# Kernel optimization log

Hardware: AMD Instinct MI355X
Metric: run time of the kernel (lower is better)

Reference implementation:

```python
import jax, jax.numpy as jnp
import numpy as np

T, B, I, H = 512, 64, 256, 512

def setup_inputs() -> dict:
    key = jax.random.key(0)
    ks = jax.random.split(key, 5)
    s = 0.1  # matches uniform(-0.1, 0.1) init scale
    return {
        "x": jax.random.normal(ks[0], (T, B, I), dtype=jnp.float32),
        "weight_ih": jax.random.uniform(ks[1], (H, I), dtype=jnp.float32, minval=-s, maxval=s),
        "weight_hh": jax.random.uniform(ks[2], (H, H), dtype=jnp.float32, minval=-s, maxval=s),
        "bias_ih": jax.random.uniform(ks[3], (H,), dtype=jnp.float32, minval=-s, maxval=s),
        "bias_hh": jax.random.uniform(ks[4], (H,), dtype=jnp.float32, minval=-s, maxval=s),
    }

def reference(x, weight_ih, weight_hh, bias_ih, bias_hh):
    # Precompute input contribution for all timesteps in one big GEMM: [T,B,H]
    xw = jnp.einsum('tbi,hi->tbh', x, weight_ih) + bias_ih + bias_hh
    h0 = jnp.zeros((x.shape[1], weight_hh.shape[0]), dtype=x.dtype)

    def step(h, xw_t):
        h = jax.nn.relu(xw_t + h @ weight_hh.T)
        return h, h

    h_final, output = jax.lax.scan(step, h0, xw)
    return output, h_final
```

## Files before the change

### kernel.cpp

```cpp
#include <hip/hip_runtime.h>

#define T_DIM 512
#define B_DIM 64
#define I_DIM 256
#define H_DIM 512
#define BH_DIM (B_DIM * H_DIM)

__global__ __launch_bounds__(256) void xw_gemm(
    const float* __restrict__ x, const float* __restrict__ wih,
    const float* __restrict__ bih, const float* __restrict__ bhh,
    float* __restrict__ out) {
  __shared__ float xs[32][68];
  __shared__ float ws[32][68];

  const int m_base = blockIdx.y * 64;
  const int n_base = blockIdx.x * 64;
  const int tid = threadIdx.x;
  const int tn = tid & 15;
  const int tm = tid >> 4;
  const int lr = tid >> 3;
  const int lk = (tid & 7) << 2;

  float acc[4][4];
#pragma unroll
  for (int i = 0; i < 4; i++)
#pragma unroll
    for (int j = 0; j < 4; j++) acc[i][j] = 0.f;

  for (int kc = 0; kc < I_DIM; kc += 32) {
    __syncthreads();
    const float4 xv0 = *(const float4*)&x[(size_t)(m_base + lr) * I_DIM + kc + lk];
    const float4 xv1 = *(const float4*)&x[(size_t)(m_base + lr + 32) * I_DIM + kc + lk];
    const float4 wv0 = *(const float4*)&wih[(size_t)(n_base + lr) * I_DIM + kc + lk];
    const float4 wv1 = *(const float4*)&wih[(size_t)(n_base + lr + 32) * I_DIM + kc + lk];
    xs[lk + 0][lr] = xv0.x; xs[lk + 1][lr] = xv0.y;
    xs[lk + 2][lr] = xv0.z; xs[lk + 3][lr] = xv0.w;
    xs[lk + 0][lr + 32] = xv1.x; xs[lk + 1][lr + 32] = xv1.y;
    xs[lk + 2][lr + 32] = xv1.z; xs[lk + 3][lr + 32] = xv1.w;
    ws[lk + 0][lr] = wv0.x; ws[lk + 1][lr] = wv0.y;
    ws[lk + 2][lr] = wv0.z; ws[lk + 3][lr] = wv0.w;
    ws[lk + 0][lr + 32] = wv1.x; ws[lk + 1][lr + 32] = wv1.y;
    ws[lk + 2][lr + 32] = wv1.z; ws[lk + 3][lr + 32] = wv1.w;
    __syncthreads();

#pragma unroll
    for (int k = 0; k < 32; k++) {
      const float4 a = *(const float4*)&xs[k][tm * 4];
      const float4 b = *(const float4*)&ws[k][tn * 4];
      acc[0][0] = fmaf(a.x, b.x, acc[0][0]); acc[0][1] = fmaf(a.x, b.y, acc[0][1]);
      acc[0][2] = fmaf(a.x, b.z, acc[0][2]); acc[0][3] = fmaf(a.x, b.w, acc[0][3]);
      acc[1][0] = fmaf(a.y, b.x, acc[1][0]); acc[1][1] = fmaf(a.y, b.y, acc[1][1]);
      acc[1][2] = fmaf(a.y, b.z, acc[1][2]); acc[1][3] = fmaf(a.y, b.w, acc[1][3]);
      acc[2][0] = fmaf(a.z, b.x, acc[2][0]); acc[2][1] = fmaf(a.z, b.y, acc[2][1]);
      acc[2][2] = fmaf(a.z, b.z, acc[2][2]); acc[2][3] = fmaf(a.z, b.w, acc[2][3]);
      acc[3][0] = fmaf(a.w, b.x, acc[3][0]); acc[3][1] = fmaf(a.w, b.y, acc[3][1]);
      acc[3][2] = fmaf(a.w, b.z, acc[3][2]); acc[3][3] = fmaf(a.w, b.w, acc[3][3]);
    }
  }

  const int n0 = n_base + tn * 4;
  float4 bias;
  bias.x = bih[n0 + 0] + bhh[n0 + 0];
  bias.y = bih[n0 + 1] + bhh[n0 + 1];
  bias.z = bih[n0 + 2] + bhh[n0 + 2];
  bias.w = bih[n0 + 3] + bhh[n0 + 3];
#pragma unroll
  for (int mi = 0; mi < 4; mi++) {
    const int m = m_base + tm * 4 + mi;
    float4 o;
    o.x = acc[mi][0] + bias.x; o.y = acc[mi][1] + bias.y;
    o.z = acc[mi][2] + bias.z; o.w = acc[mi][3] + bias.w;
    *(float4*)&out[(size_t)m * H_DIM + n0] = o;
  }
}

__global__ __launch_bounds__(512, 2) void rnn_scan_tag2(
    const float* __restrict__ whh, float* __restrict__ out,
    unsigned long long* __restrict__ stage) {
  __shared__ __align__(16) float hbuf[2][H_DIM];

  const int b   = blockIdx.x & 63;
  const int rb  = blockIdx.x >> 6;
  const int tid = threadIdx.x;
  const int rg  = tid >> 4;
  const int cg  = tid & 15;
  const int j0  = rb * 128 + rg * 4;

  const int pj = (tid < rb * 128) ? tid : tid + 128;

  float4 w[4][8];
#pragma unroll
  for (int r = 0; r < 4; r++) {
    const float4* wr = (const float4*)(whh + (size_t)(j0 + r) * H_DIM);
#pragma unroll
    for (int i = 0; i < 8; i++) w[r][i] = wr[i * 16 + cg];
  }

  float* __restrict__ outb = out + (size_t)b * H_DIM;
  unsigned long long* __restrict__ stg0 = stage + (size_t)b * H_DIM;
  unsigned long long* __restrict__ stg1 = stage + (size_t)(64 + b) * H_DIM;

  float hlast = 0.f;
  if (cg < 4) {
    const int j = j0 + cg;
    float v = fmaxf(outb[j], 0.f);
    union { float f; unsigned int u; } cv; cv.f = v;
    __hip_atomic_store(&stg0[j], (unsigned long long)cv.u,
                       __ATOMIC_RELAXED, __HIP_MEMORY_SCOPE_AGENT);
    outb[j] = v;
    hbuf[0][j] = v;
    hlast = v;
  }

  for (int t = 1; t < T_DIM; t++) {
    const int p = (t - 1) & 1;
    float* hb = hbuf[p];
    float* o_t = outb + (size_t)t * BH_DIM;

    float xw = 0.f;
    if (cg < 4) xw = o_t[j0 + cg];

    if (tid < 384) {
      unsigned long long* slot = (p ? stg1 : stg0) + pj;
      const unsigned int want = (unsigned int)(t - 1);
      unsigned long long v;
      do {
        v = __hip_atomic_load(slot, __ATOMIC_RELAXED, __HIP_MEMORY_SCOPE_AGENT);
      } while ((unsigned int)(v >> 32) != want);
      union { unsigned int u; float f; } cv; cv.u = (unsigned int)v;
      hb[pj] = cv.f;
    }

    __syncthreads();

    float a0 = 0.f, a1 = 0.f, a2 = 0.f, a3 = 0.f;
#pragma unroll
    for (int i = 0; i < 8; i++) {
      const float4 hv = ((const float4*)hb)[i * 16 + cg];
      a0 = fmaf(w[0][i].x, hv.x, a0); a0 = fmaf(w[0][i].y, hv.y, a0);
      a0 = fmaf(w[0][i].z, hv.z, a0); a0 = fmaf(w[0][i].w, hv.w, a0);
      a1 = fmaf(w[1][i].x, hv.x, a1); a1 = fmaf(w[1][i].y, hv.y, a1);
      a1 = fmaf(w[1][i].z, hv.z, a1); a1 = fmaf(w[1][i].w, hv.w, a1);
      a2 = fmaf(w[2][i].x, hv.x, a2); a2 = fmaf(w[2][i].y, hv.y, a2);
      a2 = fmaf(w[2][i].z, hv.z, a2); a2 = fmaf(w[2][i].w, hv.w, a2);
      a3 = fmaf(w[3][i].x, hv.x, a3); a3 = fmaf(w[3][i].y, hv.y, a3);
      a3 = fmaf(w[3][i].z, hv.z, a3); a3 = fmaf(w[3][i].w, hv.w, a3);
    }
#pragma unroll
    for (int m = 1; m <= 8; m <<= 1) {
      a0 += __shfl_xor(a0, m, 64);
      a1 += __shfl_xor(a1, m, 64);
      a2 += __shfl_xor(a2, m, 64);
      a3 += __shfl_xor(a3, m, 64);
    }

    if (cg < 4) {
      const float acc = (cg == 0) ? a0 : (cg == 1) ? a1 : (cg == 2) ? a2 : a3;
      const float h = fmaxf(acc + xw, 0.f);
      const int j = j0 + cg;
      union { float f; unsigned int u; } cv; cv.f = h;
      const unsigned long long tag = (unsigned long long)(unsigned int)t << 32;
      unsigned long long* sb = (t & 1) ? stg1 : stg0;
      __hip_atomic_store(&sb[j], tag | cv.u,
                         __ATOMIC_RELAXED, __HIP_MEMORY_SCOPE_AGENT);
      o_t[j] = h;
      hbuf[t & 1][j] = h;
      hlast = h;
    }
  }

  if (cg < 4) {
    out[(size_t)T_DIM * BH_DIM + (size_t)b * H_DIM + j0 + cg] = hlast;
  }
}

extern "C" void kernel_launch(void* const* d_in, const int* in_sizes, int n_in,
                              void* d_out, int out_size, void* d_ws, size_t ws_size,
                              hipStream_t stream) {
  const float* x   = (const float*)d_in[0];
  const float* wih = (const float*)d_in[1];
  const float* whh = (const float*)d_in[2];
  const float* bih = (const float*)d_in[3];
  const float* bhh = (const float*)d_in[4];
  float* out = (float*)d_out;
  unsigned long long* stage = (unsigned long long*)d_ws;

  dim3 g1(H_DIM / 64, (T_DIM * B_DIM) / 64);
  xw_gemm<<<g1, 256, 0, stream>>>(x, wih, bih, bhh, out);

  rnn_scan_tag2<<<256, 512, 0, stream>>>(whh, out, stage);
}
```

Baseline: 1.037 ms.

## Fuse input projection GEMM into persistent RNN scan kernel

Removes the separate xw GEMM kernel and computes each step's input projection inside the scan kernel. The block's W_ih slice is staged in LDS, and x rows are prefetched two steps ahead into a triple buffer. The x·W_ih dot product is issued before the spin-wait on the previous hidden state, so it can hide behind the inter-block synchronisation latency. This saves a kernel launch and the global round-trip of the xw tensor. In exchange it uses about 135KB of LDS per block and adds arithmetic inside every step.

Result: faster. 939.1 us (-9.5%).

```diff
diff --git a/kernel.cpp b/kernel.cpp
--- a/kernel.cpp
+++ b/kernel.cpp
@@ -6,78 +6,14 @@
 #define H_DIM 512
 #define BH_DIM (B_DIM * H_DIM)
 
-__global__ __launch_bounds__(256) void xw_gemm(
+__global__ __launch_bounds__(512, 2) void rnn_fused(
     const float* __restrict__ x, const float* __restrict__ wih,
-    const float* __restrict__ bih, const float* __restrict__ bhh,
-    float* __restrict__ out) {
-  __shared__ float xs[32][68];
-  __shared__ float ws[32][68];
-
-  const int m_base = blockIdx.y * 64;
-  const int n_base = blockIdx.x * 64;
-  const int tid = threadIdx.x;
-  const int tn = tid & 15;
-  const int tm = tid >> 4;
-  const int lr = tid >> 3;
-  const int lk = (tid & 7) << 2;
-
-  float acc[4][4];
-#pragma unroll
-  for (int i = 0; i < 4; i++)
-#pragma unroll
-    for (int j = 0; j < 4; j++) acc[i][j] = 0.f;
-
-  for (int kc = 0; kc < I_DIM; kc += 32) {
-    __syncthreads();
-    const float4 xv0 = *(const float4*)&x[(size_t)(m_base + lr) * I_DIM + kc + lk];
-    const float4 xv1 = *(const float4*)&x[(size_t)(m_base + lr + 32) * I_DIM + kc + lk];
-    const float4 wv0 = *(const float4*)&wih[(size_t)(n_base + lr) * I_DIM + kc + lk];
-    const float4 wv1 = *(const float4*)&wih[(size_t)(n_base + lr + 32) * I_DIM + kc + lk];
-    xs[lk + 0][lr] = xv0.x; xs[lk + 1][lr] = xv0.y;
-    xs[lk + 2][lr] = xv0.z; xs[lk + 3][lr] = xv0.w;
-    xs[lk + 0][lr + 32] = xv1.x; xs[lk + 1][lr + 32] = xv1.y;
-    xs[lk + 2][lr + 32] = xv1.z; xs[lk + 3][lr + 32] = xv1.w;
-    ws[lk + 0][lr] = wv0.x; ws[lk + 1][lr] = wv0.y;
-    ws[lk + 2][lr] = wv0.z; ws[lk + 3][lr] = wv0.w;
-    ws[lk + 0][lr + 32] = wv1.x; ws[lk + 1][lr + 32] = wv1.y;
-    ws[lk + 2][lr + 32] = wv1.z; ws[lk + 3][lr + 32] = wv1.w;
-    __syncthreads();
-
-#pragma unroll
-    for (int k = 0; k < 32; k++) {
-      const float4 a = *(const float4*)&xs[k][tm * 4];
-      const float4 b = *(const float4*)&ws[k][tn * 4];
-      acc[0][0] = fmaf(a.x, b.x, acc[0][0]); acc[0][1] = fmaf(a.x, b.y, acc[0][1]);
-      acc[0][2] = fmaf(a.x, b.z, acc[0][2]); acc[0][3] = fmaf(a.x, b.w, acc[0][3]);
-      acc[1][0] = fmaf(a.y, b.x, acc[1][0]); acc[1][1] = fmaf(a.y, b.y, acc[1][1]);
-      acc[1][2] = fmaf(a.y, b.z, acc[1][2]); acc[1][3] = fmaf(a.y, b.w, acc[1][3]);
-      acc[2][0] = fmaf(a.z, b.x, acc[2][0]); acc[2][1] = fmaf(a.z, b.y, acc[2][1]);
-      acc[2][2] = fmaf(a.z, b.z, acc[2][2]); acc[2][3] = fmaf(a.z, b.w, acc[2][3]);
-      acc[3][0] = fmaf(a.w, b.x, acc[3][0]); acc[3][1] = fmaf(a.w, b.y, acc[3][1]);
-      acc[3][2] = fmaf(a.w, b.z, acc[3][2]); acc[3][3] = fmaf(a.w, b.w, acc[3][3]);
-    }
-  }
-
-  const int n0 = n_base + tn * 4;
-  float4 bias;
-  bias.x = bih[n0 + 0] + bhh[n0 + 0];
-  bias.y = bih[n0 + 1] + bhh[n0 + 1];
-  bias.z = bih[n0 + 2] + bhh[n0 + 2];
-  bias.w = bih[n0 + 3] + bhh[n0 + 3];
-#pragma unroll
-  for (int mi = 0; mi < 4; mi++) {
-    const int m = m_base + tm * 4 + mi;
-    float4 o;
-    o.x = acc[mi][0] + bias.x; o.y = acc[mi][1] + bias.y;
-    o.z = acc[mi][2] + bias.z; o.w = acc[mi][3] + bias.w;
-    *(float4*)&out[(size_t)m * H_DIM + n0] = o;
-  }
-}
-
-__global__ __launch_bounds__(512, 2) void rnn_scan_tag2(
-    const float* __restrict__ whh, float* __restrict__ out,
+    const float* __restrict__ whh, const float* __restrict__ bih,
+    const float* __restrict__ bhh, float* __restrict__ out,
     unsigned long long* __restrict__ stage) {
+  __shared__ __align__(16) float4 wihs4[128 * 64];
   __shared__ __align__(16) float hbuf[2][H_DIM];
+  __shared__ __align__(16) float4 xbuf4[3 * 64];
 
   const int b   = blockIdx.x & 63;
   const int rb  = blockIdx.x >> 6;
@@ -96,20 +32,73 @@
     for (int i = 0; i < 8; i++) w[r][i] = wr[i * 16 + cg];
   }
 
+  {
+    const float4* wg = (const float4*)(wih + (size_t)rb * 128 * I_DIM);
+#pragma unroll
+    for (int q = 0; q < 16; q++) {
+      const int idx = q * 512 + tid;
+      wihs4[idx] = wg[idx];
+    }
+  }
+
+  const float4* xg = (const float4*)x;
+  if (tid < 64) {
+    xbuf4[0 * 64 + tid] = xg[((size_t)0 * B_DIM + b) * 64 + tid];
+    xbuf4[1 * 64 + tid] = xg[((size_t)1 * B_DIM + b) * 64 + tid];
+  }
+
+  float bias = 0.f;
+  if (cg < 4) bias = bih[j0 + cg] + bhh[j0 + cg];
+
   float* __restrict__ outb = out + (size_t)b * H_DIM;
   unsigned long long* __restrict__ stg0 = stage + (size_t)b * H_DIM;
   unsigned long long* __restrict__ stg1 = stage + (size_t)(64 + b) * H_DIM;
 
+  __syncthreads();
+
   float hlast = 0.f;
-  if (cg < 4) {
-    const int j = j0 + cg;
-    float v = fmaxf(outb[j], 0.f);
-    union { float f; unsigned int u; } cv; cv.f = v;
-    __hip_atomic_store(&stg0[j], (unsigned long long)cv.u,
-                       __ATOMIC_RELAXED, __HIP_MEMORY_SCOPE_AGENT);
-    outb[j] = v;
-    hbuf[0][j] = v;
-    hlast = v;
+
+  {
+    float b0 = 0.f, b1 = 0.f, b2 = 0.f, b3 = 0.f;
+    const float4* xb = &xbuf4[0];
+    const float4* wr = &wihs4[(rg * 4) * 64];
+#pragma unroll
+    for (int i = 0; i < 4; i++) {
+      const float4 xv = xb[i * 16 + cg];
+      const float4 q0 = wr[0 * 64 + i * 16 + cg];
+      const float4 q1 = wr[1 * 64 + i * 16 + cg];
+      const float4 q2 = wr[2 * 64 + i * 16 + cg];
+      const float4 q3 = wr[3 * 64 + i * 16 + cg];
+      b0 = fmaf(q0.x, xv.x, b0); b0 = fmaf(q0.y, xv.y, b0);
+      b0 = fmaf(q0.z, xv.z, b0); b0 = fmaf(q0.w, xv.w, b0);
+      b1 = fmaf(q1.x, xv.x, b1); b1 = fmaf(q1.y, xv.y, b1);
+      b1 = fmaf(q1.z, xv.z, b1); b1 = fmaf(q1.w, xv.w, b1);
+      b2 = fmaf(q2.x, xv.x, b2); b2 = fmaf(q2.y, xv.y, b2);
+      b2 = fmaf(q2.z, xv.z, b2); b2 = fmaf(q2.w, xv.w, b2);
+      b3 = fmaf(q3.x, xv.x, b3); b3 = fmaf(q3.y, xv.y, b3);
+      b3 = fmaf(q3.z, xv.z, b3); b3 = fmaf(q3.w, xv.w, b3);
+    }
+#pragma unroll
+    for (int m = 1; m <= 8; m <<= 1) {
+      b0 += __shfl_xor(b0, m, 64);
+      b1 += __shfl_xor(b1, m, 64);
+      b2 += __shfl_xor(b2, m, 64);
+      b3 += __shfl_xor(b3, m, 64);
+    }
+    if (cg < 4) {
+      const float acc = (cg == 0) ? b0 : (cg == 1) ? b1 : (cg == 2) ? b2 : b3;
+      const float h = fmaxf(acc + bias, 0.f);
+      const int j = j0 + cg;
+      union { float f; unsigned int u; } cv; cv.f = h;
+      __hip_atomic_store(&stg0[j], (unsigned long long)cv.u,
+                         __ATOMIC_RELAXED, __HIP_MEMORY_SCOPE_AGENT);
+      outb[j] = h;
+      hbuf[0][j] = h;
+      hlast = h;
+    }
+    if (tid < 64) {
+      xbuf4[2 * 64 + tid] = xg[((size_t)2 * B_DIM + b) * 64 + tid];
+    }
   }
 
   for (int t = 1; t < T_DIM; t++) {
@@ -117,8 +106,31 @@
     float* hb = hbuf[p];
     float* o_t = outb + (size_t)t * BH_DIM;
 
-    float xw = 0.f;
-    if (cg < 4) xw = o_t[j0 + cg];
+    float b0 = 0.f, b1 = 0.f, b2 = 0.f, b3 = 0.f;
+    {
+      const float4* xb = &xbuf4[(t % 3) * 64];
+      const float4* wr = &wihs4[(rg * 4) * 64];
+#pragma unroll
+      for (int i = 0; i < 4; i++) {
+        const float4 xv = xb[i * 16 + cg];
+        const float4 q0 = wr[0 * 64 + i * 16 + cg];
+        const float4 q1 = wr[1 * 64 + i * 16 + cg];
+        const float4 q2 = wr[2 * 64 + i * 16 + cg];
+        const float4 q3 = wr[3 * 64 + i * 16 + cg];
+        b0 = fmaf(q0.x, xv.x, b0); b0 = fmaf(q0.y, xv.y, b0);
+        b0 = fmaf(q0.z, xv.z, b0); b0 = fmaf(q0.w, xv.w, b0);
+        b1 = fmaf(q1.x, xv.x, b1); b1 = fmaf(q1.y, xv.y, b1);
+        b1 = fmaf(q1.z, xv.z, b1); b1 = fmaf(q1.w, xv.w, b1);
+        b2 = fmaf(q2.x, xv.x, b2); b2 = fmaf(q2.y, xv.y, b2);
+        b2 = fmaf(q2.z, xv.z, b2); b2 = fmaf(q2.w, xv.w, b2);
+        b3 = fmaf(q3.x, xv.x, b3); b3 = fmaf(q3.y, xv.y, b3);
+        b3 = fmaf(q3.z, xv.z, b3); b3 = fmaf(q3.w, xv.w, b3);
+      }
+    }
+
+    float4 xpf = make_float4(0.f, 0.f, 0.f, 0.f);
+    const bool do_pf = (tid < 64) && (t + 2 < T_DIM);
+    if (do_pf) xpf = xg[((size_t)(t + 2) * B_DIM + b) * 64 + tid];
 
     if (tid < 384) {
       unsigned long long* slot = (p ? stg1 : stg0) + pj;
@@ -133,7 +145,9 @@
 
     __syncthreads();
 
-    float a0 = 0.f, a1 = 0.f, a2 = 0.f, a3 = 0.f;
+    if (do_pf) xbuf4[((t + 2) % 3) * 64 + tid] = xpf;
+
+    float a0 = b0, a1 = b1, a2 = b2, a3 = b3;
 #pragma unroll
     for (int i = 0; i < 8; i++) {
       const float4 hv = ((const float4*)hb)[i * 16 + cg];
@@ -156,7 +170,7 @@
 
     if (cg < 4) {
       const float acc = (cg == 0) ? a0 : (cg == 1) ? a1 : (cg == 2) ? a2 : a3;
-      const float h = fmaxf(acc + xw, 0.f);
+      const float h = fmaxf(acc + bias, 0.f);
       const int j = j0 + cg;
       union { float f; unsigned int u; } cv; cv.f = h;
       const unsigned long long tag = (unsigned long long)(unsigned int)t << 32;
@@ -185,8 +199,5 @@
   float* out = (float*)d_out;
   unsigned long long* stage = (unsigned long long*)d_ws;
 
-  dim3 g1(H_DIM / 64, (T_DIM * B_DIM) / 64);
-  xw_gemm<<<g1, 256, 0, stream>>>(x, wih, bih, bhh, out);
-
-  rnn_scan_tag2<<<256, 512, 0, stream>>>(whh, out, stage);
+  rnn_fused<<<256, 512, 0, stream>>>(x, wih, whh, bih, bhh, out, stage);
 }
```
